# Optimization experiments

Hardware: AMD Instinct MI355X
Metric: run time of the kernel (lower is better)

The kernel has to match this reference:

```python
import jax, jax.numpy as jnp
import numpy as np
import math

B, N, EPG = 128, 512, 8192            # graphs, nodes/graph, edges/graph
E = B * EPG
DIN, H, DOUT = 128, 128, 10
RATIO = 0.8
K1 = math.ceil(RATIO * N)             # 410 nodes/graph after pool 1
K2 = math.ceil(RATIO * K1)            # 328 nodes/graph after pool 2
EPS = 1e-5


def setup_inputs() -> dict:
    key = jax.random.key(0)
    ks = jax.random.split(key, 16)
    x = jax.random.normal(ks[0], (B * N, DIN), jnp.float32)
    gid = jnp.repeat(jnp.arange(B, dtype=jnp.int32), EPG)
    src = jax.random.randint(ks[1], (E,), 0, N, dtype=jnp.int32) + gid * N
    dst = jax.random.randint(ks[2], (E,), 0, N, dtype=jnp.int32) + gid * N
    edge_index = jnp.stack([src, dst])

    def w(k, shape, fan_in):
        return jax.random.uniform(k, shape, jnp.float32, -1.0, 1.0) / np.sqrt(fan_in).astype(np.float32)

    return {
        "x": x, "edge_index": edge_index,
        "conv1_W": w(ks[3], (DIN, H), DIN), "conv1_b": jnp.zeros((H,), jnp.float32),
        "conv2_W": w(ks[4], (H, H), H),     "conv2_b": jnp.zeros((H,), jnp.float32),
        "score1_W": w(ks[5], (H, 1), H),    "score1_b": jnp.zeros((1,), jnp.float32),
        "score2_W": w(ks[6], (H, 1), H),    "score2_b": jnp.zeros((1,), jnp.float32),
        "bn1_g": jnp.ones((H,), jnp.float32), "bn1_b": jnp.zeros((H,), jnp.float32),
        "bn1_m": 0.1 * jax.random.normal(ks[7], (H,), jnp.float32),
        "bn1_v": jax.random.uniform(ks[8], (H,), jnp.float32, 0.5, 1.5),
        "bn2_g": jnp.ones((H,), jnp.float32), "bn2_b": jnp.zeros((H,), jnp.float32),
        "bn2_m": 0.1 * jax.random.normal(ks[9], (H,), jnp.float32),
        "bn2_v": jax.random.uniform(ks[10], (H,), jnp.float32, 0.5, 1.5),
        "lin0_W": w(ks[11], (DOUT, DIN), DIN), "lin0_b": jnp.zeros((DOUT,), jnp.float32),
        "lin1_W": w(ks[12], (DOUT, H), H),     "lin1_b": jnp.zeros((DOUT,), jnp.float32),
        "lin2_W": w(ks[13], (DOUT, H), H),     "lin2_b": jnp.zeros((DOUT,), jnp.float32),
    }


def gcn(h_in, src, dst, emask, W, b, n):
    # PyG GCNConv: self-loops + symmetric normalization D^-1/2 (A+I) D^-1/2 (XW) + b
    deg = jnp.ones((n,), h_in.dtype).at[dst].add(emask)      # self-loop counts as 1
    dinv = jax.lax.rsqrt(deg)
    coef = (dinv[src] * dinv[dst] * emask)[:, None]          # masked-out edges -> 0
    h = h_in @ W
    agg = jnp.zeros_like(h).at[dst].add(h[src] * coef)
    return agg + h * (dinv * dinv)[:, None] + b              # self-loop message + bias


def sag_pool(x, score, src, dst, emask, n_per, k):
    # topk per graph (equal-sized graphs -> static shapes), x <- x[perm]*tanh(score[perm])
    idx = jax.lax.top_k(score.reshape(B, n_per), k)[1]                      # [B,k]
    perm = (idx.astype(jnp.int32) + (jnp.arange(B, dtype=jnp.int32) * n_per)[:, None]).reshape(-1)
    xn = x[perm] * jnp.tanh(score[perm])[:, None]
    # filter_adj: remap surviving nodes, mask edges touching dropped nodes
    remap = jnp.full((B * n_per,), -1, jnp.int32).at[perm].set(jnp.arange(B * k, dtype=jnp.int32))
    s2, d2 = remap[src], remap[dst]
    em2 = emask * (s2 >= 0).astype(emask.dtype) * (d2 >= 0).astype(emask.dtype)
    return xn, jnp.maximum(s2, 0), jnp.maximum(d2, 0), em2


def bn_relu(x, g, b, m, v):
    # eval-mode BatchNorm1d followed by ReLU
    return jax.nn.relu(g * (x - m) * jax.lax.rsqrt(v + EPS) + b)


def reference(x, edge_index, conv1_W, conv1_b, conv2_W, conv2_b,
              score1_W, score1_b, score2_W, score2_b,
              bn1_g, bn1_b, bn1_m, bn1_v, bn2_g, bn2_b, bn2_m, bn2_v,
              lin0_W, lin0_b, lin1_W, lin1_b, lin2_W, lin2_b):
    src, dst = edge_index[0], edge_index[1]
    emask = jnp.ones((E,), x.dtype)
    hidden = [(x, N)]
    # layer 0: GCNConv -> SAGPool -> BN -> ReLU
    h = gcn(x, src, dst, emask, conv1_W, conv1_b, B * N)
    s = gcn(h, src, dst, emask, score1_W, score1_b, B * N)[:, 0]
    h, src, dst, emask = sag_pool(h, s, src, dst, emask, N, K1)
    h = bn_relu(h, bn1_g, bn1_b, bn1_m, bn1_v)
    hidden.append((h, K1))
    # layer 1
    h = gcn(h, src, dst, emask, conv2_W, conv2_b, B * K1)
    s = gcn(h, src, dst, emask, score2_W, score2_b, B * K1)[:, 0]
    h, src, dst, emask = sag_pool(h, s, src, dst, emask, K1, K2)
    h = bn_relu(h, bn2_g, bn2_b, bn2_m, bn2_v)
    hidden.append((h, K2))
    # jumping-knowledge readout: global_add_pool each rep, per-layer linear, sum (dropout eval = id)
    lins = [(lin0_W, lin0_b), (lin1_W, lin1_b), (lin2_W, lin2_b)]
    out = jnp.zeros((B, DOUT), x.dtype)
    for (hh, n_per), (W, bb) in zip(hidden, lins):
        pooled = hh.reshape(B, n_per, -1).sum(axis=1)   # global_add_pool (segment sum)
        out = out + pooled @ W.T + bb
    return out
```

## Files before the change

### kernel.cpp

```cpp
#include <hip/hip_runtime.h>

#define Bg   128
#define NPG  512
#define EPGc 8192
#define Etot (Bg*EPGc)
#define DOUTc 10
#define K1c  410
#define K2c  328
#define N0c  (Bg*NPG)
#define N1c  (Bg*K1c)
#define N2c  (Bg*K2c)
#define EPSc 1e-5f

typedef __attribute__((ext_vector_type(8))) short s8v;
typedef __attribute__((ext_vector_type(4))) float f4v;

static __device__ __forceinline__ unsigned short bf_rne(float x) {
  unsigned u = __float_as_uint(x);
  u += 0x7FFFu + ((u >> 16) & 1u);
  return (unsigned short)(u >> 16);
}
static __device__ __forceinline__ float bf_f(unsigned short h) {
  return __uint_as_float(((unsigned)h) << 16);
}

static __global__ __launch_bounds__(512) void k_prep0(const int* __restrict__ src,
                                                      const int* __restrict__ dst,
                                                      const float* __restrict__ W1,
                                                      const float* __restrict__ W2,
                                                      unsigned short* __restrict__ pk,
                                                      float* __restrict__ dinv,
                                                      int* __restrict__ rp,
                                                      int2* __restrict__ e2,
                                                      float* __restrict__ pooled) {
  __shared__ int    cnt[NPG];
  __shared__ float  sdv[NPG];
  __shared__ int    srp[NPG];
  __shared__ int    sbuf[512];
  int g = blockIdx.x, tid = threadIdx.x;
  cnt[tid] = 0;
  if (tid < 128) {
    pooled[g * 128 + tid] = 0.f;
    pooled[Bg * 128 + g * 128 + tid] = 0.f;
    pooled[2 * Bg * 128 + g * 128 + tid] = 0.f;
  }
  if (tid < 256) {
    int i = g * 256 + tid;
    const float* W = (i < 16384) ? W1 : W2;
    unsigned short* d = pk + ((i < 16384) ? 0 : 32768);
    int ii = i & 16383;
    int grp = ii >> 9, lane = (ii >> 3) & 63, j = ii & 7;
    int kk = grp >> 3, t = grp & 7;
    int k = kk * 32 + (lane >> 4) * 8 + j;
    int n = t * 16 + (lane & 15);
    float w = W[k * 128 + n];
    unsigned short hi = bf_rne(w);
    d[ii] = hi;
    d[16384 + ii] = bf_rne(w - bf_f(hi));
  }
  __syncthreads();
  const int* sp = src + (size_t)g * EPGc;
  const int* dp = dst + (size_t)g * EPGc;
  for (int e = tid; e < EPGc; e += 512) atomicAdd(&cnt[dp[e] - g * NPG], 1);
  __syncthreads();
  int c = cnt[tid];
  float dv = 1.0f / sqrtf(1.0f + (float)c);
  sdv[tid] = dv;
  dinv[g * NPG + tid] = dv;
  sbuf[tid] = c;
  __syncthreads();
  for (int off = 1; off < 512; off <<= 1) {
    int t = (tid >= off) ? sbuf[tid - off] : 0;
    __syncthreads();
    sbuf[tid] += t;
    __syncthreads();
  }
  srp[tid] = sbuf[tid] - c;
  rp[g * (NPG + 1) + tid] = sbuf[tid] - c;
  if (tid == 511) rp[g * (NPG + 1) + NPG] = sbuf[511];
  cnt[tid] = 0;
  __syncthreads();
  for (int e = tid; e < EPGc; e += 512) {
    int s = sp[e], d = dp[e];
    int dl = d - g * NPG;
    int pos = srp[dl] + atomicAdd(&cnt[dl], 1);
    e2[(size_t)g * EPGc + pos] =
        make_int2(s, __float_as_int(sdv[s - g * NPG] * sdv[dl]));
  }
}

static __global__ __launch_bounds__(256) void k_gemm3(const float* __restrict__ X,
                                                      const unsigned short* __restrict__ pk,
                                                      float* __restrict__ Y,
                                                      float* __restrict__ p0) {
  __shared__ unsigned short wl[32768];
  int tid = threadIdx.x;
  for (int i = tid; i < 4096; i += 256) ((int4*)wl)[i] = ((const int4*)pk)[i];
  int wv = tid >> 6, lane = tid & 63;
  int q = lane >> 4, m16 = lane & 15;
  size_t row = (size_t)blockIdx.x * 64 + wv * 16 + m16;
  float* pg = p0 ? (p0 + (size_t)(blockIdx.x >> 3) * 128) : nullptr;
  s8v ahi[4], alo[4];
#pragma unroll
  for (int kk = 0; kk < 4; ++kk) {
    const float* xr = X + row * 128 + kk * 32 + q * 8;
    float4 a0 = *(const float4*)xr;
    float4 a1 = *(const float4*)(xr + 4);
    float av[8] = {a0.x, a0.y, a0.z, a0.w, a1.x, a1.y, a1.z, a1.w};
    if (pg) {
#pragma unroll
      for (int j = 0; j < 8; ++j) {
        float v = av[j];
        v += __shfl_xor(v, 1, 64); v += __shfl_xor(v, 2, 64);
        v += __shfl_xor(v, 4, 64); v += __shfl_xor(v, 8, 64);
        if (m16 == 0) atomicAdd(&pg[kk * 32 + q * 8 + j], v);
      }
    }
    union { unsigned short u[8]; s8v v; } H, L;
#pragma unroll
    for (int j = 0; j < 8; ++j) {
      unsigned short h = bf_rne(av[j]);
      H.u[j] = h;
      L.u[j] = bf_rne(av[j] - bf_f(h));
    }
    ahi[kk] = H.v; alo[kk] = L.v;
  }
  __syncthreads();
  int orow0 = blockIdx.x * 64 + wv * 16 + q * 4;
#pragma unroll
  for (int t = 0; t < 8; ++t) {
    f4v acc = {0.f, 0.f, 0.f, 0.f};
#pragma unroll
    for (int kk = 0; kk < 4; ++kk) {
      s8v bhi = *(const s8v*)&wl[(kk * 8 + t) * 512 + lane * 8];
      s8v blo = *(const s8v*)&wl[16384 + (kk * 8 + t) * 512 + lane * 8];
      acc = __builtin_amdgcn_mfma_f32_16x16x32_bf16(ahi[kk], bhi, acc, 0, 0, 0);
      acc = __builtin_amdgcn_mfma_f32_16x16x32_bf16(alo[kk], bhi, acc, 0, 0, 0);
      acc = __builtin_amdgcn_mfma_f32_16x16x32_bf16(ahi[kk], blo, acc, 0, 0, 0);
    }
#pragma unroll
    for (int r = 0; r < 4; ++r)
      Y[(size_t)(orow0 + r) * 128 + t * 16 + m16] = acc[r];
  }
}

template <int NPER, int RG>
static __global__ __launch_bounds__(256) void k_agg3(const float* __restrict__ h0,
                                                     const float* __restrict__ dinv,
                                                     const float* __restrict__ bias,
                                                     const int* __restrict__ rp,
                                                     const int2* __restrict__ e2,
                                                     const float* __restrict__ sw,
                                                     float* __restrict__ h1,
                                                     float* __restrict__ spre) {
  int tid = threadIdx.x;
  int hw = tid >> 5, l = tid & 31;
  int b = blockIdx.x;
  int xcd = b & 7, slot = b >> 3;
  int g = xcd * 16 + (slot & 15);
  int rowgrp = slot >> 4;
  int li = rowgrp * 8 + hw;
  if (li >= NPER) return;
  int j = g * NPER + li;
  const int* rpg = rp + g * (NPER + 1);
  int start = rpg[li], end = rpg[li + 1];
  const int2* ep = e2 + (size_t)g * EPGc;
  float di = dinv[j];
  float sc = di * di;
  float4 acc = *(const float4*)&h0[(size_t)j * 128 + l * 4];
  float4 bb = ((const float4*)bias)[l];
  acc.x = acc.x * sc + bb.x; acc.y = acc.y * sc + bb.y;
  acc.z = acc.z * sc + bb.z; acc.w = acc.w * sc + bb.w;
  int e = start;
  for (; e + 4 <= end; e += 4) {
    int2 p0 = ep[e], p1 = ep[e + 1], p2 = ep[e + 2], p3 = ep[e + 3];
    float4 v0 = *(const float4*)&h0[(size_t)p0.x * 128 + l * 4];
    float4 v1 = *(const float4*)&h0[(size_t)p1.x * 128 + l * 4];
    float4 v2 = *(const float4*)&h0[(size_t)p2.x * 128 + l * 4];
    float4 v3 = *(const float4*)&h0[(size_t)p3.x * 128 + l * 4];
    float c0 = __int_as_float(p0.y), c1 = __int_as_float(p1.y);
    float c2 = __int_as_float(p2.y), c3 = __int_as_float(p3.y);
    acc.x += v0.x * c0 + v1.x * c1 + v2.x * c2 + v3.x * c3;
    acc.y += v0.y * c0 + v1.y * c1 + v2.y * c2 + v3.y * c3;
    acc.z += v0.z * c0 + v1.z * c1 + v2.z * c2 + v3.z * c3;
    acc.w += v0.w * c0 + v1.w * c1 + v2.w * c2 + v3.w * c3;
  }
  for (; e < end; ++e) {
    int2 pp = ep[e];
    float c = __int_as_float(pp.y);
    float4 v = *(const float4*)&h0[(size_t)pp.x * 128 + l * 4];
    acc.x += v.x * c; acc.y += v.y * c; acc.z += v.z * c; acc.w += v.w * c;
  }
  ((float4*)&h1[(size_t)j * 128])[l] = acc;
  float4 w4 = ((const float4*)sw)[l];
  float pr = acc.x * w4.x + acc.y * w4.y + acc.z * w4.z + acc.w * w4.w;
#pragma unroll
  for (int off = 16; off; off >>= 1) pr += __shfl_xor(pr, off, 64);
  if (l == 0) spre[j] = pr;
}

template <int NPER, int K>
static __global__ __launch_bounds__(512) void k_repool(const float* __restrict__ spre,
                                                       const float* __restrict__ dinv,
                                                       const float* __restrict__ sb,
                                                       const int* __restrict__ rp,
                                                       const int* __restrict__ src,
                                                       const int* __restrict__ dst,
                                                       int* __restrict__ perm,
                                                       float* __restrict__ tsel,
                                                       float* __restrict__ dinv2,
                                                       int* __restrict__ rp2,
                                                       int2* __restrict__ e2) {
  __shared__ float ss[NPER];
  __shared__ float sc[512];
  __shared__ int   sidx[512];
  __shared__ short rmp[NPER];
  __shared__ int   cnt[K];
  __shared__ float sdv[K];
  __shared__ int   srp[K];
  __shared__ int   sbuf[512];
  int g = blockIdx.x, tid = threadIdx.x;
  if (tid < NPER) { ss[tid] = spre[g * NPER + tid]; rmp[tid] = -1; }
  __syncthreads();
  if (tid < NPER) {
    const int* rpg = rp + g * (NPER + 1);
    int st = rpg[tid], en = rpg[tid + 1];
    const int2* ep = e2 + (size_t)g * EPGc;
    float di = dinv[g * NPER + tid];
    float acc = ss[tid] * di * di + sb[0];
    int e = st;
    for (; e + 4 <= en; e += 4) {
      int2 p0 = ep[e], p1 = ep[e + 1], p2 = ep[e + 2], p3 = ep[e + 3];
      acc += ss[p0.x - g * NPER] * __int_as_float(p0.y) +
             ss[p1.x - g * NPER] * __int_as_float(p1.y) +
             ss[p2.x - g * NPER] * __int_as_float(p2.y) +
             ss[p3.x - g * NPER] * __int_as_float(p3.y);
    }
    for (; e < en; ++e) { int2 pp = ep[e]; acc += ss[pp.x - g * NPER] * __int_as_float(pp.y); }
    sc[tid] = acc;
  } else {
    sc[tid] = -3.402823466e38f;
  }
  sidx[tid] = tid;
  __syncthreads();
  for (int kk = 2; kk <= 512; kk <<= 1) {
    for (int j = kk >> 1; j > 0; j >>= 1) {
      int i = tid, p = i ^ j;
      if (p > i) {
        bool up = ((i & kk) == 0);
        float si = sc[i], sp2 = sc[p];
        if (up ? (si < sp2) : (si > sp2)) {
          sc[i] = sp2; sc[p] = si;
          int t = sidx[i]; sidx[i] = sidx[p]; sidx[p] = t;
        }
      }
      __syncthreads();
    }
  }
  if (tid < K) {
    perm[g * K + tid] = g * NPER + sidx[tid];
    tsel[g * K + tid] = tanhf(sc[tid]);
    rmp[sidx[tid]] = (short)tid;
    cnt[tid] = 0;
  }
  __syncthreads();
  const int* sp = src + (size_t)g * EPGc;
  const int* dp = dst + (size_t)g * EPGc;
  for (int e = tid; e < EPGc; e += 512) {
    int s = rmp[sp[e] - g * NPER];
    int d = rmp[dp[e] - g * NPER];
    if ((s | d) >= 0) atomicAdd(&cnt[d], 1);
  }
  __syncthreads();
  int c = (tid < K) ? cnt[tid] : 0;
  if (tid < K) {
    float dv = 1.0f / sqrtf(1.0f + (float)c);
    sdv[tid] = dv;
    dinv2[g * K + tid] = dv;
  }
  sbuf[tid] = c;
  __syncthreads();
  for (int off = 1; off < 512; off <<= 1) {
    int t = (tid >= off) ? sbuf[tid - off] : 0;
    __syncthreads();
    sbuf[tid] += t;
    __syncthreads();
  }
  if (tid < K) { srp[tid] = sbuf[tid] - c; rp2[g * (K + 1) + tid] = sbuf[tid] - c; cnt[tid] = 0; }
  if (tid == 511) rp2[g * (K + 1) + K] = sbuf[511];
  __syncthreads();
  for (int e = tid; e < EPGc; e += 512) {
    int s = rmp[sp[e] - g * NPER];
    int d = rmp[dp[e] - g * NPER];
    if ((s | d) >= 0) {
      int pos = srp[d] + atomicAdd(&cnt[d], 1);
      e2[(size_t)g * EPGc + pos] = make_int2(g * K + s, __float_as_int(sdv[s] * sdv[d]));
    }
  }
}

template <int NPER, int K>
static __global__ __launch_bounds__(512) void k_topk2(const float* __restrict__ spre,
                                                      const float* __restrict__ dinv2,
                                                      const float* __restrict__ sb,
                                                      const int* __restrict__ rp2,
                                                      const int2* __restrict__ e2,
                                                      int* __restrict__ perm,
                                                      float* __restrict__ tsel) {
  __shared__ float ss[NPER];
  __shared__ float sc[512];
  __shared__ int   sidx[512];
  int g = blockIdx.x, tid = threadIdx.x;
  if (tid < NPER) ss[tid] = spre[g * NPER + tid];
  __syncthreads();
  if (tid < NPER) {
    const int* rpg = rp2 + g * (NPER + 1);
    int st = rpg[tid], en = rpg[tid + 1];
    const int2* ep = e2 + (size_t)g * EPGc;
    float di = dinv2[g * NPER + tid];
    float acc = ss[tid] * di * di + sb[0];
    int e = st;
    for (; e + 4 <= en; e += 4) {
      int2 p0 = ep[e], p1 = ep[e + 1], p2 = ep[e + 2], p3 = ep[e + 3];
      acc += ss[p0.x - g * NPER] * __int_as_float(p0.y) +
             ss[p1.x - g * NPER] * __int_as_float(p1.y) +
             ss[p2.x - g * NPER] * __int_as_float(p2.y) +
             ss[p3.x - g * NPER] * __int_as_float(p3.y);
    }
    for (; e < en; ++e) { int2 pp = ep[e]; acc += ss[pp.x - g * NPER] * __int_as_float(pp.y); }
    sc[tid] = acc;
  } else {
    sc[tid] = -3.402823466e38f;
  }
  sidx[tid] = tid;
  __syncthreads();
  for (int kk = 2; kk <= 512; kk <<= 1) {
    for (int j = kk >> 1; j > 0; j >>= 1) {
      int i = tid, p = i ^ j;
      if (p > i) {
        bool up = ((i & kk) == 0);
        float si = sc[i], sp2 = sc[p];
        if (up ? (si < sp2) : (si > sp2)) {
          sc[i] = sp2; sc[p] = si;
          int t = sidx[i]; sidx[i] = sidx[p]; sidx[p] = t;
        }
      }
      __syncthreads();
    }
  }
  if (tid < K) {
    perm[g * K + tid] = g * NPER + sidx[tid];
    tsel[g * K + tid] = tanhf(sc[tid]);
  }
}

template <int NPER, int CH, bool WXP>
static __global__ __launch_bounds__(128) void k_poolbn(const float* __restrict__ h,
                                                       const float* __restrict__ tsel,
                                                       const int* __restrict__ perm,
                                                       const float* __restrict__ gg,
                                                       const float* __restrict__ bb,
                                                       const float* __restrict__ mm,
                                                       const float* __restrict__ vv,
                                                       float* __restrict__ xp,
                                                       float* __restrict__ pooledseg) {
  int g = blockIdx.x / CH, cidx = blockIdx.x - g * CH;
  int f = threadIdx.x;
  const int rows = (NPER + CH - 1) / CH;
  int r0 = cidx * rows, r1 = min(NPER, r0 + rows);
  if (r0 >= r1) return;
  float G = gg[f], Bb = bb[f], Mm = mm[f];
  float inv = 1.0f / sqrtf(vv[f] + EPSc);
  float acc = 0.f;
  for (int r = r0; r < r1; ++r) {
    int j = g * NPER + r;
    int old = perm[j];
    float val = h[(size_t)old * 128 + f] * tsel[j];
    float o = fmaxf(G * (val - Mm) * inv + Bb, 0.f);
    if (WXP) xp[(size_t)j * 128 + f] = o;
    acc += o;
  }
  atomicAdd(&pooledseg[g * 128 + f], acc);
}

static __global__ void k_final(const float* __restrict__ pooled,
                               const float* __restrict__ w0, const float* __restrict__ b0,
                               const float* __restrict__ w1, const float* __restrict__ b1,
                               const float* __restrict__ w2, const float* __restrict__ b2,
                               float* __restrict__ out) {
  int t = blockIdx.x * 256 + threadIdx.x;
  if (t >= Bg * DOUTc) return;
  int g = t / DOUTc, o = t - g * DOUTc;
  const float* p0 = pooled + g * 128;
  const float* p1 = pooled + Bg * 128 + g * 128;
  const float* p2 = pooled + 2 * Bg * 128 + g * 128;
  float acc = b0[o] + b1[o] + b2[o];
  for (int k = 0; k < 128; ++k)
    acc += p0[k] * w0[o * 128 + k] + p1[k] * w1[o * 128 + k] + p2[k] * w2[o * 128 + k];
  out[t] = acc;
}

extern "C" void kernel_launch(void* const* d_in, const int* in_sizes, int n_in,
                              void* d_out, int out_size, void* d_ws, size_t ws_size,
                              hipStream_t stream) {
  (void)in_sizes; (void)n_in; (void)out_size; (void)ws_size;
  const float* x    = (const float*)d_in[0];
  const int*   ei   = (const int*)d_in[1];
  const int*   src0 = ei;
  const int*   dst0 = ei + Etot;
  const float* c1W = (const float*)d_in[2];  const float* c1b = (const float*)d_in[3];
  const float* c2W = (const float*)d_in[4];  const float* c2b = (const float*)d_in[5];
  const float* s1W = (const float*)d_in[6];  const float* s1b = (const float*)d_in[7];
  const float* s2W = (const float*)d_in[8];  const float* s2b = (const float*)d_in[9];
  const float* bn1g = (const float*)d_in[10]; const float* bn1b = (const float*)d_in[11];
  const float* bn1m = (const float*)d_in[12]; const float* bn1v = (const float*)d_in[13];
  const float* bn2g = (const float*)d_in[14]; const float* bn2b = (const float*)d_in[15];
  const float* bn2m = (const float*)d_in[16]; const float* bn2v = (const float*)d_in[17];
  const float* l0W = (const float*)d_in[18]; const float* l0b = (const float*)d_in[19];
  const float* l1W = (const float*)d_in[20]; const float* l1b = (const float*)d_in[21];
  const float* l2W = (const float*)d_in[22]; const float* l2b = (const float*)d_in[23];
  float* out = (float*)d_out;

  char* p = (char*)d_ws;
  auto alloc = [&](size_t bytes) { char* q = p; p += (bytes + 255) & ~(size_t)255; return q; };
  float* h0    = (float*)alloc((size_t)N0c * 128 * 4);
  float* h1    = (float*)alloc((size_t)N0c * 128 * 4);
  float* xp1   = (float*)alloc((size_t)N1c * 128 * 4);
  float* dinv  = (float*)alloc((size_t)N0c * 4);
  float* dinv2 = (float*)alloc((size_t)N1c * 4);
  int*   rp    = (int*)alloc((size_t)Bg * (NPG + 1) * 4);
  int*   rp2   = (int*)alloc((size_t)Bg * (K1c + 1) * 4);
  int2*  e2    = (int2*)alloc((size_t)Etot * 8);
  float* spre  = (float*)alloc((size_t)N0c * 4);
  float* tsel  = (float*)alloc((size_t)N1c * 4);
  int*   perm  = (int*)alloc((size_t)N1c * 4);
  unsigned short* pk = (unsigned short*)alloc((size_t)65536 * 2);
  float* pooled= (float*)alloc((size_t)3 * Bg * 128 * 4);

  dim3 b256(256), b512(512), b128(128);

  k_prep0<<<Bg, b512, 0, stream>>>(src0, dst0, c1W, c2W, pk, dinv, rp, e2, pooled);
  k_gemm3<<<N0c / 64, b256, 0, stream>>>(x, pk, h0, pooled);
  k_agg3<NPG, 64><<<128 * 64, b256, 0, stream>>>(h0, dinv, c1b, rp, e2, s1W, h1, spre);
  k_repool<NPG, K1c><<<Bg, b512, 0, stream>>>(spre, dinv, s1b, rp, src0, dst0,
                                              perm, tsel, dinv2, rp2, e2);
  k_poolbn<K1c, 16, true><<<Bg * 16, b128, 0, stream>>>(h1, tsel, perm, bn1g, bn1b,
                                                        bn1m, bn1v, xp1, pooled + Bg * 128);

  float* g1 = h0;
  float* h2 = h1;
  k_gemm3<<<N1c / 64, b256, 0, stream>>>(xp1, pk + 32768, g1, nullptr);
  k_agg3<K1c, 52><<<128 * 52, b256, 0, stream>>>(g1, dinv2, c2b, rp2, e2, s2W, h2, spre);
  k_topk2<K1c, K2c><<<Bg, b512, 0, stream>>>(spre, dinv2, s2b, rp2, e2, perm, tsel);
  k_poolbn<K2c, 16, false><<<Bg * 16, b128, 0, stream>>>(h2, tsel, perm, bn2g, bn2b,
                                                         bn2m, bn2v, nullptr,
                                                         pooled + 2 * Bg * 128);

  k_final<<<(Bg * DOUTc + 255) / 256, b256, 0, stream>>>(pooled, l0W, l0b, l1W, l1b, l2W, l2b, out);
}
```

Measured before the change: 334.8 us.

## Fuse pool-1 gather, batchnorm and ReLU into the second GEMM's input load

```diff
diff --git a/kernel.cpp b/kernel.cpp
--- a/kernel.cpp
+++ b/kernel.cpp
@@ -28,7 +28,12 @@
                                                       const int* __restrict__ dst,
                                                       const float* __restrict__ W1,
                                                       const float* __restrict__ W2,
+                                                      const float* __restrict__ bn1g,
+                                                      const float* __restrict__ bn1b,
+                                                      const float* __restrict__ bn1m,
+                                                      const float* __restrict__ bn1v,
                                                       unsigned short* __restrict__ pk,
+                                                      float2* __restrict__ bnp,
                                                       float* __restrict__ dinv,
                                                       int* __restrict__ rp,
                                                       int2* __restrict__ e2,
@@ -43,6 +48,8 @@
     pooled[g * 128 + tid] = 0.f;
     pooled[Bg * 128 + g * 128 + tid] = 0.f;
     pooled[2 * Bg * 128 + g * 128 + tid] = 0.f;
+    float sc = bn1g[tid] / sqrtf(bn1v[tid] + EPSc);
+    bnp[tid] = make_float2(sc, bn1b[tid] - bn1m[tid] * sc);
   }
   if (tid < 256) {
     int i = g * 256 + tid;
@@ -89,31 +96,59 @@
   }
 }
 
-static __global__ __launch_bounds__(256) void k_gemm3(const float* __restrict__ X,
+template <bool FUSE, int NROWG>
+static __global__ __launch_bounds__(512) void k_gemm4(const float* __restrict__ X,
                                                       const unsigned short* __restrict__ pk,
                                                       float* __restrict__ Y,
-                                                      float* __restrict__ p0) {
+                                                      float* __restrict__ pooledseg,
+                                                      const int* __restrict__ perm,
+                                                      const float* __restrict__ tsel,
+                                                      const float2* __restrict__ bnp) {
   __shared__ unsigned short wl[32768];
   int tid = threadIdx.x;
-  for (int i = tid; i < 4096; i += 256) ((int4*)wl)[i] = ((const int4*)pk)[i];
+  for (int i = tid; i < 4096; i += 512) ((int4*)wl)[i] = ((const int4*)pk)[i];
   int wv = tid >> 6, lane = tid & 63;
   int q = lane >> 4, m16 = lane & 15;
-  size_t row = (size_t)blockIdx.x * 64 + wv * 16 + m16;
-  float* pg = p0 ? (p0 + (size_t)(blockIdx.x >> 3) * 128) : nullptr;
+  int grow0 = blockIdx.x * 128 + wv * 16;
+  int row = grow0 + m16;
+  int gsel = row / NROWG;
+  bool uni = (grow0 / NROWG) == ((grow0 + 15) / NROWG);
+  const float* xr_base;
+  float tmul = 1.f;
+  if (FUSE) {
+    int old = perm[row];
+    tmul = tsel[row];
+    xr_base = X + (size_t)old * 128;
+  } else {
+    xr_base = X + (size_t)row * 128;
+  }
   s8v ahi[4], alo[4];
 #pragma unroll
   for (int kk = 0; kk < 4; ++kk) {
-    const float* xr = X + row * 128 + kk * 32 + q * 8;
+    const float* xr = xr_base + kk * 32 + q * 8;
     float4 a0 = *(const float4*)xr;
     float4 a1 = *(const float4*)(xr + 4);
     float av[8] = {a0.x, a0.y, a0.z, a0.w, a1.x, a1.y, a1.z, a1.w};
-    if (pg) {
+    if (FUSE) {
 #pragma unroll
       for (int j = 0; j < 8; ++j) {
-        float v = av[j];
-        v += __shfl_xor(v, 1, 64); v += __shfl_xor(v, 2, 64);
-        v += __shfl_xor(v, 4, 64); v += __shfl_xor(v, 8, 64);
-        if (m16 == 0) atomicAdd(&pg[kk * 32 + q * 8 + j], v);
+        float2 ss = bnp[kk * 32 + q * 8 + j];
+        av[j] = fmaxf(ss.x * (av[j] * tmul) + ss.y, 0.f);
+      }
+    }
+    if (pooledseg) {
+      if (uni) {
+#pragma unroll
+        for (int j = 0; j < 8; ++j) {
+          float v = av[j];
+          v += __shfl_xor(v, 1, 64); v += __shfl_xor(v, 2, 64);
+          v += __shfl_xor(v, 4, 64); v += __shfl_xor(v, 8, 64);
+          if (m16 == 0) atomicAdd(&pooledseg[gsel * 128 + kk * 32 + q * 8 + j], v);
+        }
+      } else {
+#pragma unroll
+        for (int j = 0; j < 8; ++j)
+          atomicAdd(&pooledseg[gsel * 128 + kk * 32 + q * 8 + j], av[j]);
       }
     }
     union { unsigned short u[8]; s8v v; } H, L;
@@ -126,7 +161,7 @@
     ahi[kk] = H.v; alo[kk] = L.v;
   }
   __syncthreads();
-  int orow0 = blockIdx.x * 64 + wv * 16 + q * 4;
+  int orow0 = grow0 + q * 4;
 #pragma unroll
   for (int t = 0; t < 8; ++t) {
     f4v acc = {0.f, 0.f, 0.f, 0.f};
@@ -354,7 +389,7 @@
   }
 }
 
-template <int NPER, int CH, bool WXP>
+template <int NPER, int CH>
 static __global__ __launch_bounds__(128) void k_poolbn(const float* __restrict__ h,
                                                        const float* __restrict__ tsel,
                                                        const int* __restrict__ perm,
@@ -362,7 +397,6 @@
                                                        const float* __restrict__ bb,
                                                        const float* __restrict__ mm,
                                                        const float* __restrict__ vv,
-                                                       float* __restrict__ xp,
                                                        float* __restrict__ pooledseg) {
   int g = blockIdx.x / CH, cidx = blockIdx.x - g * CH;
   int f = threadIdx.x;
@@ -377,7 +411,6 @@
     int old = perm[j];
     float val = h[(size_t)old * 128 + f] * tsel[j];
     float o = fmaxf(G * (val - Mm) * inv + Bb, 0.f);
-    if (WXP) xp[(size_t)j * 128 + f] = o;
     acc += o;
   }
   atomicAdd(&pooledseg[g * 128 + f], acc);
@@ -425,7 +458,6 @@
   auto alloc = [&](size_t bytes) { char* q = p; p += (bytes + 255) & ~(size_t)255; return q; };
   float* h0    = (float*)alloc((size_t)N0c * 128 * 4);
   float* h1    = (float*)alloc((size_t)N0c * 128 * 4);
-  float* xp1   = (float*)alloc((size_t)N1c * 128 * 4);
   float* dinv  = (float*)alloc((size_t)N0c * 4);
   float* dinv2 = (float*)alloc((size_t)N1c * 4);
   int*   rp    = (int*)alloc((size_t)Bg * (NPG + 1) * 4);
@@ -435,26 +467,27 @@
   float* tsel  = (float*)alloc((size_t)N1c * 4);
   int*   perm  = (int*)alloc((size_t)N1c * 4);
   unsigned short* pk = (unsigned short*)alloc((size_t)65536 * 2);
+  float2* bnp  = (float2*)alloc((size_t)128 * 8);
   float* pooled= (float*)alloc((size_t)3 * Bg * 128 * 4);
 
   dim3 b256(256), b512(512), b128(128);
 
-  k_prep0<<<Bg, b512, 0, stream>>>(src0, dst0, c1W, c2W, pk, dinv, rp, e2, pooled);
-  k_gemm3<<<N0c / 64, b256, 0, stream>>>(x, pk, h0, pooled);
+  k_prep0<<<Bg, b512, 0, stream>>>(src0, dst0, c1W, c2W, bn1g, bn1b, bn1m, bn1v,
+                                   pk, bnp, dinv, rp, e2, pooled);
+  k_gemm4<false, NPG><<<N0c / 128, b512, 0, stream>>>(x, pk, h0, pooled,
+                                                      nullptr, nullptr, nullptr);
   k_agg3<NPG, 64><<<128 * 64, b256, 0, stream>>>(h0, dinv, c1b, rp, e2, s1W, h1, spre);
   k_repool<NPG, K1c><<<Bg, b512, 0, stream>>>(spre, dinv, s1b, rp, src0, dst0,
                                               perm, tsel, dinv2, rp2, e2);
-  k_poolbn<K1c, 16, true><<<Bg * 16, b128, 0, stream>>>(h1, tsel, perm, bn1g, bn1b,
-                                                        bn1m, bn1v, xp1, pooled + Bg * 128);
 
   float* g1 = h0;
+  k_gemm4<true, K1c><<<N1c / 128, b512, 0, stream>>>(h1, pk + 32768, g1,
+                                                     pooled + Bg * 128, perm, tsel, bnp);
   float* h2 = h1;
-  k_gemm3<<<N1c / 64, b256, 0, stream>>>(xp1, pk + 32768, g1, nullptr);
   k_agg3<K1c, 52><<<128 * 52, b256, 0, stream>>>(g1, dinv2, c2b, rp2, e2, s2W, h2, spre);
   k_topk2<K1c, K2c><<<Bg, b512, 0, stream>>>(spre, dinv2, s2b, rp2, e2, perm, tsel);
-  k_poolbn<K2c, 16, false><<<Bg * 16, b128, 0, stream>>>(h2, tsel, perm, bn2g, bn2b,
-                                                         bn2m, bn2v, nullptr,
-                                                         pooled + 2 * Bg * 128);
+  k_poolbn<K2c, 16><<<Bg * 16, b128, 0, stream>>>(h2, tsel, perm, bn2g, bn2b,
+                                                  bn2m, bn2v, pooled + 2 * Bg * 128);
 
   k_final<<<(Bg * DOUTc + 255) / 256, b256, 0, stream>>>(pooled, l0W, l0b, l1W, l1b, l2W, l2b, out);
 }
```

Result: slower. 353.8 us (+5.7%).
